# Kernel tuning notes

Measured on AMD Instinct MI355X. Metric: run time of the kernel, lower is better.

Reference implementation:

```python
import jax, jax.numpy as jnp
import numpy as np

B, S, D, H = 2, 4096, 512, 8
DK = D // H  # 64

def setup_inputs() -> dict:
    key = jax.random.key(0)
    k1, k2, k3, k4 = jax.random.split(key, 4)
    return {
        "queries": jax.random.normal(k1, (B, S, D), dtype=jnp.float32),
        "keys": jax.random.normal(k2, (B, S, D), dtype=jnp.float32),
        "values": jax.random.normal(k3, (B, S, D), dtype=jnp.float32),
        "W_o": jax.random.normal(k4, (D, D), dtype=jnp.float32) * (1.0 / np.sqrt(D)),
        "b_o": jnp.zeros((D,), dtype=jnp.float32),
    }

def reference(queries, keys, values, W_o, b_o):
    b_s, nq, _ = queries.shape
    nk = keys.shape[1]
    # split heads: (b, s, h, dk) -> (b, h, s, dk)
    q = queries.reshape(b_s, nq, H, DK).transpose(0, 2, 1, 3)
    k = keys.reshape(b_s, nk, H, DK).transpose(0, 2, 1, 3)
    v = values.reshape(b_s, nk, H, DK).transpose(0, 2, 1, 3)
    # full (nq, nk) attention matrix, scaled by sqrt(d_k)
    att = jnp.einsum("bhqd,bhkd->bhqk", q, k) / np.sqrt(DK).astype(np.float32)
    att = jax.nn.softmax(att, axis=-1)  # dropout is identity at inference
    out = jnp.einsum("bhqk,bhkd->bhqd", att, v)
    out = out.transpose(0, 2, 1, 3).reshape(b_s, nq, H * DK)
    return out @ W_o + b_o
```

## Files before the change

### kernel.cpp

```cpp
#include <hip/hip_runtime.h>
#include <hip/hip_bf16.h>

#define Bn 2
#define Sn 4096
#define Dn 512
#define Hn 8
#define DKn 64

typedef __bf16 bf16x8 __attribute__((ext_vector_type(8)));
typedef float f32x16 __attribute__((ext_vector_type(16)));

static __device__ __forceinline__ unsigned short f2bf(float x) {
    __hip_bfloat16 h = __float2bfloat16(x);
    return *reinterpret_cast<unsigned short*>(&h);
}

static __device__ __forceinline__ uint2 pack4(float a, float b, float c, float d) {
    union { ushort4 u; uint2 v; } r;
    r.u.x = f2bf(a); r.u.y = f2bf(b); r.u.z = f2bf(c); r.u.w = f2bf(d);
    return r.v;
}

static __device__ __forceinline__ bf16x8 xchg_frag(uint2 pg0, uint2 pg1, int hi) {
    int sx = hi ? (int)pg0.x : (int)pg1.x;
    int sy = hi ? (int)pg0.y : (int)pg1.y;
    int rx = __shfl_xor(sx, 32);
    int ry = __shfl_xor(sy, 32);
    unsigned ox = hi ? pg1.x : pg0.x;
    unsigned oy = hi ? pg1.y : pg0.y;
    union { unsigned u[4]; bf16x8 v; } f;
    f.u[0] = hi ? (unsigned)rx : ox;
    f.u[1] = hi ? (unsigned)ry : oy;
    f.u[2] = hi ? ox : (unsigned)rx;
    f.u[3] = hi ? oy : (unsigned)ry;
    return f.v;
}

__global__ __launch_bounds__(256) void kprep_kernel(const float* __restrict__ K,
                                                    unsigned short* __restrict__ Kb) {
    const int kt = blockIdx.x, bh = blockIdx.y;
    const int b = bh >> 3, h = bh & 7;
    unsigned short* dst = Kb + ((size_t)bh * 64 + kt) * 4096;
#pragma unroll
    for (int i = 0; i < 2; ++i) {
        int c = threadIdx.x + i * 256;
        int f = c >> 6, ln = c & 63;
        int ktile = f >> 2, ks = f & 3;
        int row = ktile * 32 + (ln & 31);
        int dk = ks * 16 + (ln >> 5) * 8;
        const float* src = K + ((size_t)(b * Sn + kt * 64 + row)) * Dn + h * 64 + dk;
        float4 a0 = *(const float4*)src;
        float4 a1 = *(const float4*)(src + 4);
        ushort4 o0; o0.x = f2bf(a0.x); o0.y = f2bf(a0.y); o0.z = f2bf(a0.z); o0.w = f2bf(a0.w);
        ushort4 o1; o1.x = f2bf(a1.x); o1.y = f2bf(a1.y); o1.z = f2bf(a1.z); o1.w = f2bf(a1.w);
        *(ushort4*)(dst + c * 8) = o0;
        *(ushort4*)(dst + c * 8 + 4) = o1;
    }
}

__global__ __launch_bounds__(256) void vprep_kernel(const float* __restrict__ V,
                                                    unsigned short* __restrict__ Vb) {
    const int kt = blockIdx.x, bh = blockIdx.y;
    const int b = bh >> 3, h = bh & 7;
    unsigned short* dst = Vb + ((size_t)bh * 64 + kt) * 4096;
#pragma unroll
    for (int i = 0; i < 2; ++i) {
        int c = threadIdx.x + i * 256;
        int f = c >> 6, ln = c & 63;
        int dt = f >> 2, ks = f & 3;
        int dk = dt * 32 + (ln & 31);
        int key0 = ks * 16 + (ln >> 5) * 8;
        const float* src = V + ((size_t)(b * Sn + kt * 64 + key0)) * Dn + h * 64 + dk;
        ushort4 o0, o1;
        o0.x = f2bf(src[0 * Dn]); o0.y = f2bf(src[1 * Dn]);
        o0.z = f2bf(src[2 * Dn]); o0.w = f2bf(src[3 * Dn]);
        o1.x = f2bf(src[4 * Dn]); o1.y = f2bf(src[5 * Dn]);
        o1.z = f2bf(src[6 * Dn]); o1.w = f2bf(src[7 * Dn]);
        *(ushort4*)(dst + c * 8) = o0;
        *(ushort4*)(dst + c * 8 + 4) = o1;
    }
}

__global__ __launch_bounds__(256) void wprep_kernel(const float* __restrict__ W,
                                                    unsigned short* __restrict__ Wb) {
    int c = blockIdx.x * 256 + threadIdx.x;
    int ln = c & 63, f = c >> 6;
    int ntile = f >> 5, ks = f & 31;
    int n = ntile * 32 + (ln & 31);
    int k0 = ks * 16 + (ln >> 5) * 8;
    ushort4 o0, o1;
    o0.x = f2bf(W[(size_t)(k0 + 0) * Dn + n]); o0.y = f2bf(W[(size_t)(k0 + 1) * Dn + n]);
    o0.z = f2bf(W[(size_t)(k0 + 2) * Dn + n]); o0.w = f2bf(W[(size_t)(k0 + 3) * Dn + n]);
    o1.x = f2bf(W[(size_t)(k0 + 4) * Dn + n]); o1.y = f2bf(W[(size_t)(k0 + 5) * Dn + n]);
    o1.z = f2bf(W[(size_t)(k0 + 6) * Dn + n]); o1.w = f2bf(W[(size_t)(k0 + 7) * Dn + n]);
    *(ushort4*)(Wb + c * 8) = o0;
    *(ushort4*)(Wb + c * 8 + 4) = o1;
}

__global__ __launch_bounds__(256) void attn_kernel(
    const float* __restrict__ Q,
    const unsigned short* __restrict__ Kb,
    const unsigned short* __restrict__ Vb,
    unsigned short* __restrict__ ObA) {
    __shared__ __align__(16) unsigned short Ksh[4096];
    __shared__ __align__(16) unsigned short Vsh[4096];

    const int qt = blockIdx.x;
    const int bh = blockIdx.y;
    const int b = bh >> 3, h = bh & 7;
    const int tid = threadIdx.x;
    const int w = tid >> 6;
    const int lane = tid & 63;
    const int q = lane & 31;
    const int hi = lane >> 5;
    const int q0 = qt * 128 + w * 32;
    const float cexp = 0.18033688f;

    bf16x8 qf[4];
    {
        const float* qp = Q + ((size_t)(b * Sn + q0 + q)) * Dn + h * 64 + hi * 8;
#pragma unroll
        for (int ks = 0; ks < 4; ++ks) {
            float4 a0 = *(const float4*)(qp + ks * 16);
            float4 a1 = *(const float4*)(qp + ks * 16 + 4);
            union { unsigned short u[8]; bf16x8 v; } f;
            f.u[0] = f2bf(a0.x * cexp); f.u[1] = f2bf(a0.y * cexp);
            f.u[2] = f2bf(a0.z * cexp); f.u[3] = f2bf(a0.w * cexp);
            f.u[4] = f2bf(a1.x * cexp); f.u[5] = f2bf(a1.y * cexp);
            f.u[6] = f2bf(a1.z * cexp); f.u[7] = f2bf(a1.w * cexp);
            qf[ks] = f.v;
        }
    }

    f32x16 oacc[2];
#pragma unroll
    for (int t = 0; t < 2; ++t)
#pragma unroll
        for (int r = 0; r < 16; ++r) oacc[t][r] = 0.f;
    float l_ = 0.f;

    const unsigned short* kg = Kb + (size_t)bh * (64 * 4096);
    const unsigned short* vg = Vb + (size_t)bh * (64 * 4096);

    for (int kt = 0; kt < 64; ++kt) {
        __syncthreads();
        {
            const unsigned short* ks_ = kg + (size_t)kt * 4096;
            const unsigned short* vs_ = vg + (size_t)kt * 4096;
            uint4 k0 = *(const uint4*)(ks_ + tid * 8);
            uint4 k1 = *(const uint4*)(ks_ + 2048 + tid * 8);
            uint4 v0 = *(const uint4*)(vs_ + tid * 8);
            uint4 v1 = *(const uint4*)(vs_ + 2048 + tid * 8);
            *(uint4*)&Ksh[tid * 8] = k0;
            *(uint4*)&Ksh[2048 + tid * 8] = k1;
            *(uint4*)&Vsh[tid * 8] = v0;
            *(uint4*)&Vsh[2048 + tid * 8] = v1;
        }
        __syncthreads();

        f32x16 sacc[2];
#pragma unroll
        for (int t = 0; t < 2; ++t)
#pragma unroll
            for (int r = 0; r < 16; ++r) sacc[t][r] = 0.f;
#pragma unroll
        for (int ks = 0; ks < 4; ++ks) {
            bf16x8 ka0 = *(const bf16x8*)&Ksh[(0 * 4 + ks) * 512 + lane * 8];
            bf16x8 ka1 = *(const bf16x8*)&Ksh[(1 * 4 + ks) * 512 + lane * 8];
            sacc[0] = __builtin_amdgcn_mfma_f32_32x32x16_bf16(ka0, qf[ks], sacc[0], 0, 0, 0);
            sacc[1] = __builtin_amdgcn_mfma_f32_32x32x16_bf16(ka1, qf[ks], sacc[1], 0, 0, 0);
        }

        float p[2][16];
#pragma unroll
        for (int t = 0; t < 2; ++t) {
            float s0 = 0.f, s1 = 0.f;
#pragma unroll
            for (int r = 0; r < 16; r += 2) {
                float e0 = __builtin_amdgcn_exp2f(sacc[t][r]);
                float e1 = __builtin_amdgcn_exp2f(sacc[t][r + 1]);
                p[t][r] = e0; p[t][r + 1] = e1;
                s0 += e0; s1 += e1;
            }
            l_ += s0 + s1;
        }

#pragma unroll
        for (int kp = 0; kp < 4; ++kp) {
            const int c = kp >> 1, k2 = kp & 1;
            uint2 pg0 = pack4(p[c][8 * k2 + 0], p[c][8 * k2 + 1], p[c][8 * k2 + 2], p[c][8 * k2 + 3]);
            uint2 pg1 = pack4(p[c][8 * k2 + 4], p[c][8 * k2 + 5], p[c][8 * k2 + 6], p[c][8 * k2 + 7]);
            bf16x8 pb = xchg_frag(pg0, pg1, hi);
            bf16x8 va0 = *(const bf16x8*)&Vsh[(0 * 4 + kp) * 512 + lane * 8];
            bf16x8 va1 = *(const bf16x8*)&Vsh[(1 * 4 + kp) * 512 + lane * 8];
            oacc[0] = __builtin_amdgcn_mfma_f32_32x32x16_bf16(va0, pb, oacc[0], 0, 0, 0);
            oacc[1] = __builtin_amdgcn_mfma_f32_32x32x16_bf16(va1, pb, oacc[1], 0, 0, 0);
        }
    }

    l_ += __shfl_xor(l_, 32);
    const float li = 1.f / l_;
    const int gm = b * 128 + qt * 4 + w;
#pragma unroll
    for (int ksg = 0; ksg < 4; ++ksg) {
        const int dt = ksg >> 1, k2 = ksg & 1;
        uint2 pg0 = pack4(oacc[dt][8 * k2 + 0] * li, oacc[dt][8 * k2 + 1] * li,
                          oacc[dt][8 * k2 + 2] * li, oacc[dt][8 * k2 + 3] * li);
        uint2 pg1 = pack4(oacc[dt][8 * k2 + 4] * li, oacc[dt][8 * k2 + 5] * li,
                          oacc[dt][8 * k2 + 6] * li, oacc[dt][8 * k2 + 7] * li);
        bf16x8 frag = xchg_frag(pg0, pg1, hi);
        union { bf16x8 v; uint4 u; } fu; fu.v = frag;
        *(uint4*)&ObA[((size_t)(gm * 32 + h * 4 + ksg) * 64 + lane) * 8] = fu.u;
    }
}

__global__ __launch_bounds__(256) void proj_kernel(
    const unsigned short* __restrict__ ObA,
    const unsigned short* __restrict__ Wb,
    const float* __restrict__ bias,
    float* __restrict__ out) {
    __shared__ __align__(16) unsigned short Ash[8192];
    __shared__ __align__(16) unsigned short Wsh[4096];

    const int mt = blockIdx.x;
    const int nt = blockIdx.y;
    const int tid = threadIdx.x;
    const int w = tid >> 6;
    const int lane = tid & 63;
    const int q = lane & 31;
    const int hi = lane >> 5;

    f32x16 acc[2];
#pragma unroll
    for (int t = 0; t < 2; ++t)
#pragma unroll
        for (int r = 0; r < 16; ++r) acc[t][r] = 0.f;

    for (int kt = 0; kt < 8; ++kt) {
        __syncthreads();
#pragma unroll
        for (int i = 0; i < 4; ++i) {
            int ci = (tid >> 6) + i * 4;
            int ml = ci >> 2, ksl = ci & 3;
            *(uint4*)&Ash[ci * 512 + lane * 8] =
                *(const uint4*)(ObA + (((size_t)(mt * 4 + ml) * 32 + kt * 4 + ksl) * 64 + lane) * 8);
        }
#pragma unroll
        for (int i = 0; i < 2; ++i) {
            int ci = (tid >> 6) + i * 4;
            int ntl = ci >> 2, ksl = ci & 3;
            *(uint4*)&Wsh[ci * 512 + lane * 8] =
                *(const uint4*)(Wb + (((size_t)(nt * 2 + ntl) * 32 + kt * 4 + ksl) * 64 + lane) * 8);
        }
        __syncthreads();

#pragma unroll
        for (int ks = 0; ks < 4; ++ks) {
            bf16x8 a  = *(const bf16x8*)&Ash[(w * 4 + ks) * 512 + lane * 8];
            bf16x8 b0 = *(const bf16x8*)&Wsh[(0 * 4 + ks) * 512 + lane * 8];
            bf16x8 b1 = *(const bf16x8*)&Wsh[(4 + ks) * 512 + lane * 8];
            acc[0] = __builtin_amdgcn_mfma_f32_32x32x16_bf16(a, b0, acc[0], 0, 0, 0);
            acc[1] = __builtin_amdgcn_mfma_f32_32x32x16_bf16(a, b1, acc[1], 0, 0, 0);
        }
    }

#pragma unroll
    for (int ntl = 0; ntl < 2; ++ntl) {
        int col = nt * 64 + ntl * 32 + q;
        float bv = bias[col];
#pragma unroll
        for (int reg = 0; reg < 16; ++reg) {
            int row = mt * 128 + w * 32 + (reg & 3) + 8 * (reg >> 2) + 4 * hi;
            out[(size_t)row * Dn + col] = acc[ntl][reg] + bv;
        }
    }
}

extern "C" void kernel_launch(void* const* d_in, const int* in_sizes, int n_in,
                              void* d_out, int out_size, void* d_ws, size_t ws_size,
                              hipStream_t stream) {
    const float* Q = (const float*)d_in[0];
    const float* K = (const float*)d_in[1];
    const float* V = (const float*)d_in[2];
    const float* W = (const float*)d_in[3];
    const float* bo = (const float*)d_in[4];
    float* out = (float*)d_out;

    char* ws = (char*)d_ws;
    unsigned short* Kb  = (unsigned short*)(ws);
    unsigned short* Vb  = (unsigned short*)(ws + 8388608);
    unsigned short* Wb  = (unsigned short*)(ws + 16777216);
    unsigned short* ObA = (unsigned short*)(ws + 17301504);

    kprep_kernel<<<dim3(64, 16), 256, 0, stream>>>(K, Kb);
    vprep_kernel<<<dim3(64, 16), 256, 0, stream>>>(V, Vb);
    wprep_kernel<<<128, 256, 0, stream>>>(W, Wb);
    attn_kernel<<<dim3(32, 16), 256, 0, stream>>>(Q, Kb, Vb, ObA);
    proj_kernel<<<dim3(64, 8), 256, 0, stream>>>(ObA, Wb, bo, out);
}
```

Baseline: 218.2 us.

## Split attention KV loop across two wave groups, fuse prep kernels, cheaper bf16 pack

The attention kernel now runs 512 threads per block, with two halves of four waves each. Each half processes half of the key tiles into its own LDS buffers, and the partial output accumulators and row sums are combined through LDS at the end. This doubles the waves working on each query tile, aiming at better latency hiding. The three prep kernels are merged into one launch to save launch overhead. Float-to-bf16 conversion now uses add-0x8000 plus a perm instruction; this is round-half-up rather than round-to-nearest-even and does not handle NaN specially.

```diff
diff --git a/kernel.cpp b/kernel.cpp
--- a/kernel.cpp
+++ b/kernel.cpp
@@ -5,29 +5,24 @@
 #define Sn 4096
 #define Dn 512
 #define Hn 8
-#define DKn 64
 
 typedef __bf16 bf16x8 __attribute__((ext_vector_type(8)));
 typedef float f32x16 __attribute__((ext_vector_type(16)));
 
-static __device__ __forceinline__ unsigned short f2bf(float x) {
-    __hip_bfloat16 h = __float2bfloat16(x);
-    return *reinterpret_cast<unsigned short*>(&h);
-}
-
-static __device__ __forceinline__ uint2 pack4(float a, float b, float c, float d) {
-    union { ushort4 u; uint2 v; } r;
-    r.u.x = f2bf(a); r.u.y = f2bf(b); r.u.z = f2bf(c); r.u.w = f2bf(d);
-    return r.v;
-}
-
-static __device__ __forceinline__ bf16x8 xchg_frag(uint2 pg0, uint2 pg1, int hi) {
-    int sx = hi ? (int)pg0.x : (int)pg1.x;
-    int sy = hi ? (int)pg0.y : (int)pg1.y;
+static __device__ __forceinline__ unsigned pk2(float a, float b) {
+    unsigned ua = __float_as_uint(a) + 0x8000u;
+    unsigned ub = __float_as_uint(b) + 0x8000u;
+    return __builtin_amdgcn_perm(ub, ua, 0x07060302u);
+}
+
+static __device__ __forceinline__ bf16x8 xchg2(unsigned g0x, unsigned g0y,
+                                               unsigned g1x, unsigned g1y, int hi) {
+    int sx = hi ? (int)g0x : (int)g1x;
+    int sy = hi ? (int)g0y : (int)g1y;
     int rx = __shfl_xor(sx, 32);
     int ry = __shfl_xor(sy, 32);
-    unsigned ox = hi ? pg1.x : pg0.x;
-    unsigned oy = hi ? pg1.y : pg0.y;
+    unsigned ox = hi ? g1x : g0x;
+    unsigned oy = hi ? g1y : g0y;
     union { unsigned u[4]; bf16x8 v; } f;
     f.u[0] = hi ? (unsigned)rx : ox;
     f.u[1] = hi ? (unsigned)ry : oy;
@@ -36,85 +31,88 @@
     return f.v;
 }
 
-__global__ __launch_bounds__(256) void kprep_kernel(const float* __restrict__ K,
-                                                    unsigned short* __restrict__ Kb) {
-    const int kt = blockIdx.x, bh = blockIdx.y;
-    const int b = bh >> 3, h = bh & 7;
-    unsigned short* dst = Kb + ((size_t)bh * 64 + kt) * 4096;
-#pragma unroll
-    for (int i = 0; i < 2; ++i) {
-        int c = threadIdx.x + i * 256;
-        int f = c >> 6, ln = c & 63;
-        int ktile = f >> 2, ks = f & 3;
-        int row = ktile * 32 + (ln & 31);
-        int dk = ks * 16 + (ln >> 5) * 8;
-        const float* src = K + ((size_t)(b * Sn + kt * 64 + row)) * Dn + h * 64 + dk;
-        float4 a0 = *(const float4*)src;
-        float4 a1 = *(const float4*)(src + 4);
-        ushort4 o0; o0.x = f2bf(a0.x); o0.y = f2bf(a0.y); o0.z = f2bf(a0.z); o0.w = f2bf(a0.w);
-        ushort4 o1; o1.x = f2bf(a1.x); o1.y = f2bf(a1.y); o1.z = f2bf(a1.z); o1.w = f2bf(a1.w);
-        *(ushort4*)(dst + c * 8) = o0;
-        *(ushort4*)(dst + c * 8 + 4) = o1;
-    }
-}
-
-__global__ __launch_bounds__(256) void vprep_kernel(const float* __restrict__ V,
-                                                    unsigned short* __restrict__ Vb) {
-    const int kt = blockIdx.x, bh = blockIdx.y;
-    const int b = bh >> 3, h = bh & 7;
-    unsigned short* dst = Vb + ((size_t)bh * 64 + kt) * 4096;
-#pragma unroll
-    for (int i = 0; i < 2; ++i) {
-        int c = threadIdx.x + i * 256;
-        int f = c >> 6, ln = c & 63;
-        int dt = f >> 2, ks = f & 3;
-        int dk = dt * 32 + (ln & 31);
-        int key0 = ks * 16 + (ln >> 5) * 8;
-        const float* src = V + ((size_t)(b * Sn + kt * 64 + key0)) * Dn + h * 64 + dk;
-        ushort4 o0, o1;
-        o0.x = f2bf(src[0 * Dn]); o0.y = f2bf(src[1 * Dn]);
-        o0.z = f2bf(src[2 * Dn]); o0.w = f2bf(src[3 * Dn]);
-        o1.x = f2bf(src[4 * Dn]); o1.y = f2bf(src[5 * Dn]);
-        o1.z = f2bf(src[6 * Dn]); o1.w = f2bf(src[7 * Dn]);
-        *(ushort4*)(dst + c * 8) = o0;
-        *(ushort4*)(dst + c * 8 + 4) = o1;
-    }
-}
-
-__global__ __launch_bounds__(256) void wprep_kernel(const float* __restrict__ W,
-                                                    unsigned short* __restrict__ Wb) {
-    int c = blockIdx.x * 256 + threadIdx.x;
-    int ln = c & 63, f = c >> 6;
-    int ntile = f >> 5, ks = f & 31;
-    int n = ntile * 32 + (ln & 31);
-    int k0 = ks * 16 + (ln >> 5) * 8;
-    ushort4 o0, o1;
-    o0.x = f2bf(W[(size_t)(k0 + 0) * Dn + n]); o0.y = f2bf(W[(size_t)(k0 + 1) * Dn + n]);
-    o0.z = f2bf(W[(size_t)(k0 + 2) * Dn + n]); o0.w = f2bf(W[(size_t)(k0 + 3) * Dn + n]);
-    o1.x = f2bf(W[(size_t)(k0 + 4) * Dn + n]); o1.y = f2bf(W[(size_t)(k0 + 5) * Dn + n]);
-    o1.z = f2bf(W[(size_t)(k0 + 6) * Dn + n]); o1.w = f2bf(W[(size_t)(k0 + 7) * Dn + n]);
-    *(ushort4*)(Wb + c * 8) = o0;
-    *(ushort4*)(Wb + c * 8 + 4) = o1;
-}
-
-__global__ __launch_bounds__(256) void attn_kernel(
+__global__ __launch_bounds__(256) void prep_kernel(
+    const float* __restrict__ K, const float* __restrict__ V, const float* __restrict__ W,
+    unsigned short* __restrict__ Kb, unsigned short* __restrict__ Vb,
+    unsigned short* __restrict__ Wb) {
+    const int vb = blockIdx.x;
+    const int tid = threadIdx.x;
+    if (vb < 1024) {
+        const int kt = vb & 63, bh = vb >> 6;
+        const int b = bh >> 3, h = bh & 7;
+        unsigned short* dst = Kb + ((size_t)bh * 64 + kt) * 4096;
+#pragma unroll
+        for (int i = 0; i < 2; ++i) {
+            int c = tid + i * 256;
+            int f = c >> 6, ln = c & 63;
+            int ktile = f >> 2, ks = f & 3;
+            int row = ktile * 32 + (ln & 31);
+            int dk = ks * 16 + (ln >> 5) * 8;
+            const float* src = K + ((size_t)(b * Sn + kt * 64 + row)) * Dn + h * 64 + dk;
+            float4 a0 = *(const float4*)src;
+            float4 a1 = *(const float4*)(src + 4);
+            uint4 o;
+            o.x = pk2(a0.x, a0.y); o.y = pk2(a0.z, a0.w);
+            o.z = pk2(a1.x, a1.y); o.w = pk2(a1.z, a1.w);
+            *(uint4*)(dst + c * 8) = o;
+        }
+    } else if (vb < 2048) {
+        const int u = vb - 1024;
+        const int kt = u & 63, bh = u >> 6;
+        const int b = bh >> 3, h = bh & 7;
+        unsigned short* dst = Vb + ((size_t)bh * 64 + kt) * 4096;
+#pragma unroll
+        for (int i = 0; i < 2; ++i) {
+            int c = tid + i * 256;
+            int f = c >> 6, ln = c & 63;
+            int dt = f >> 2, ks = f & 3;
+            int dk = dt * 32 + (ln & 31);
+            int key0 = ks * 16 + (ln >> 5) * 8;
+            const float* src = V + ((size_t)(b * Sn + kt * 64 + key0)) * Dn + h * 64 + dk;
+            uint4 o;
+            o.x = pk2(src[0 * Dn], src[1 * Dn]); o.y = pk2(src[2 * Dn], src[3 * Dn]);
+            o.z = pk2(src[4 * Dn], src[5 * Dn]); o.w = pk2(src[6 * Dn], src[7 * Dn]);
+            *(uint4*)(dst + c * 8) = o;
+        }
+    } else {
+        int c = (vb - 2048) * 256 + tid;
+        int ln = c & 63, f = c >> 6;
+        int ntile = f >> 5, ks = f & 31;
+        int n = ntile * 32 + (ln & 31);
+        int k0 = ks * 16 + (ln >> 5) * 8;
+        uint4 o;
+        o.x = pk2(W[(size_t)(k0 + 0) * Dn + n], W[(size_t)(k0 + 1) * Dn + n]);
+        o.y = pk2(W[(size_t)(k0 + 2) * Dn + n], W[(size_t)(k0 + 3) * Dn + n]);
+        o.z = pk2(W[(size_t)(k0 + 4) * Dn + n], W[(size_t)(k0 + 5) * Dn + n]);
+        o.w = pk2(W[(size_t)(k0 + 6) * Dn + n], W[(size_t)(k0 + 7) * Dn + n]);
+        *(uint4*)(Wb + c * 8) = o;
+    }
+}
+
+__global__ __launch_bounds__(512, 4) void attn_kernel(
     const float* __restrict__ Q,
     const unsigned short* __restrict__ Kb,
     const unsigned short* __restrict__ Vb,
     unsigned short* __restrict__ ObA) {
-    __shared__ __align__(16) unsigned short Ksh[4096];
-    __shared__ __align__(16) unsigned short Vsh[4096];
+    __shared__ __align__(16) unsigned short KV[16384];
+    __shared__ float Lsh[4][64];
 
     const int qt = blockIdx.x;
     const int bh = blockIdx.y;
     const int b = bh >> 3, h = bh & 7;
     const int tid = threadIdx.x;
-    const int w = tid >> 6;
+    const int wg = tid >> 6;
+    const int half = wg >> 2;
+    const int w4 = wg & 3;
     const int lane = tid & 63;
     const int q = lane & 31;
     const int hi = lane >> 5;
-    const int q0 = qt * 128 + w * 32;
+    const int q0 = qt * 128 + w4 * 32;
+    const int th = tid & 255;
     const float cexp = 0.18033688f;
+
+    unsigned short* Kbuf = KV + half * 4096;
+    unsigned short* Vbuf = KV + 8192 + half * 4096;
 
     bf16x8 qf[4];
     {
@@ -123,94 +121,115 @@
         for (int ks = 0; ks < 4; ++ks) {
             float4 a0 = *(const float4*)(qp + ks * 16);
             float4 a1 = *(const float4*)(qp + ks * 16 + 4);
-            union { unsigned short u[8]; bf16x8 v; } f;
-            f.u[0] = f2bf(a0.x * cexp); f.u[1] = f2bf(a0.y * cexp);
-            f.u[2] = f2bf(a0.z * cexp); f.u[3] = f2bf(a0.w * cexp);
-            f.u[4] = f2bf(a1.x * cexp); f.u[5] = f2bf(a1.y * cexp);
-            f.u[6] = f2bf(a1.z * cexp); f.u[7] = f2bf(a1.w * cexp);
+            union { unsigned u[4]; bf16x8 v; } f;
+            f.u[0] = pk2(a0.x * cexp, a0.y * cexp);
+            f.u[1] = pk2(a0.z * cexp, a0.w * cexp);
+            f.u[2] = pk2(a1.x * cexp, a1.y * cexp);
+            f.u[3] = pk2(a1.z * cexp, a1.w * cexp);
             qf[ks] = f.v;
         }
     }
 
+    f32x16 zf;
+#pragma unroll
+    for (int r = 0; r < 16; ++r) zf[r] = 0.f;
     f32x16 oacc[2];
-#pragma unroll
-    for (int t = 0; t < 2; ++t)
-#pragma unroll
-        for (int r = 0; r < 16; ++r) oacc[t][r] = 0.f;
+    oacc[0] = zf; oacc[1] = zf;
     float l_ = 0.f;
 
-    const unsigned short* kg = Kb + (size_t)bh * (64 * 4096);
-    const unsigned short* vg = Vb + (size_t)bh * (64 * 4096);
-
-    for (int kt = 0; kt < 64; ++kt) {
+    const size_t tbase = ((size_t)bh * 64 + half * 32) * 4096;
+    const unsigned short* kg = Kb + tbase;
+    const unsigned short* vg = Vb + tbase;
+
+    for (int it = 0; it < 32; ++it) {
         __syncthreads();
         {
-            const unsigned short* ks_ = kg + (size_t)kt * 4096;
-            const unsigned short* vs_ = vg + (size_t)kt * 4096;
-            uint4 k0 = *(const uint4*)(ks_ + tid * 8);
-            uint4 k1 = *(const uint4*)(ks_ + 2048 + tid * 8);
-            uint4 v0 = *(const uint4*)(vs_ + tid * 8);
-            uint4 v1 = *(const uint4*)(vs_ + 2048 + tid * 8);
-            *(uint4*)&Ksh[tid * 8] = k0;
-            *(uint4*)&Ksh[2048 + tid * 8] = k1;
-            *(uint4*)&Vsh[tid * 8] = v0;
-            *(uint4*)&Vsh[2048 + tid * 8] = v1;
+            const unsigned short* ks_ = kg + (size_t)it * 4096;
+            const unsigned short* vs_ = vg + (size_t)it * 4096;
+            uint4 k0v = *(const uint4*)(ks_ + th * 8);
+            uint4 k1v = *(const uint4*)(ks_ + 2048 + th * 8);
+            uint4 v0v = *(const uint4*)(vs_ + th * 8);
+            uint4 v1v = *(const uint4*)(vs_ + 2048 + th * 8);
+            *(uint4*)&Kbuf[th * 8] = k0v;
+            *(uint4*)&Kbuf[2048 + th * 8] = k1v;
+            *(uint4*)&Vbuf[th * 8] = v0v;
+            *(uint4*)&Vbuf[2048 + th * 8] = v1v;
         }
         __syncthreads();
 
-        f32x16 sacc[2];
-#pragma unroll
-        for (int t = 0; t < 2; ++t)
-#pragma unroll
-            for (int r = 0; r < 16; ++r) sacc[t][r] = 0.f;
-#pragma unroll
-        for (int ks = 0; ks < 4; ++ks) {
-            bf16x8 ka0 = *(const bf16x8*)&Ksh[(0 * 4 + ks) * 512 + lane * 8];
-            bf16x8 ka1 = *(const bf16x8*)&Ksh[(1 * 4 + ks) * 512 + lane * 8];
-            sacc[0] = __builtin_amdgcn_mfma_f32_32x32x16_bf16(ka0, qf[ks], sacc[0], 0, 0, 0);
-            sacc[1] = __builtin_amdgcn_mfma_f32_32x32x16_bf16(ka1, qf[ks], sacc[1], 0, 0, 0);
-        }
-
-        float p[2][16];
 #pragma unroll
         for (int t = 0; t < 2; ++t) {
+            bf16x8 ka = *(const bf16x8*)&Kbuf[(t * 4 + 0) * 512 + lane * 8];
+            f32x16 sa = __builtin_amdgcn_mfma_f32_32x32x16_bf16(ka, qf[0], zf, 0, 0, 0);
+#pragma unroll
+            for (int ks = 1; ks < 4; ++ks) {
+                ka = *(const bf16x8*)&Kbuf[(t * 4 + ks) * 512 + lane * 8];
+                sa = __builtin_amdgcn_mfma_f32_32x32x16_bf16(ka, qf[ks], sa, 0, 0, 0);
+            }
+            float e[16];
             float s0 = 0.f, s1 = 0.f;
 #pragma unroll
             for (int r = 0; r < 16; r += 2) {
-                float e0 = __builtin_amdgcn_exp2f(sacc[t][r]);
-                float e1 = __builtin_amdgcn_exp2f(sacc[t][r + 1]);
-                p[t][r] = e0; p[t][r + 1] = e1;
-                s0 += e0; s1 += e1;
+                e[r] = __builtin_amdgcn_exp2f(sa[r]);
+                e[r + 1] = __builtin_amdgcn_exp2f(sa[r + 1]);
+                s0 += e[r]; s1 += e[r + 1];
             }
             l_ += s0 + s1;
-        }
-
-#pragma unroll
-        for (int kp = 0; kp < 4; ++kp) {
-            const int c = kp >> 1, k2 = kp & 1;
-            uint2 pg0 = pack4(p[c][8 * k2 + 0], p[c][8 * k2 + 1], p[c][8 * k2 + 2], p[c][8 * k2 + 3]);
-            uint2 pg1 = pack4(p[c][8 * k2 + 4], p[c][8 * k2 + 5], p[c][8 * k2 + 6], p[c][8 * k2 + 7]);
-            bf16x8 pb = xchg_frag(pg0, pg1, hi);
-            bf16x8 va0 = *(const bf16x8*)&Vsh[(0 * 4 + kp) * 512 + lane * 8];
-            bf16x8 va1 = *(const bf16x8*)&Vsh[(1 * 4 + kp) * 512 + lane * 8];
-            oacc[0] = __builtin_amdgcn_mfma_f32_32x32x16_bf16(va0, pb, oacc[0], 0, 0, 0);
-            oacc[1] = __builtin_amdgcn_mfma_f32_32x32x16_bf16(va1, pb, oacc[1], 0, 0, 0);
-        }
-    }
-
-    l_ += __shfl_xor(l_, 32);
-    const float li = 1.f / l_;
-    const int gm = b * 128 + qt * 4 + w;
-#pragma unroll
-    for (int ksg = 0; ksg < 4; ++ksg) {
-        const int dt = ksg >> 1, k2 = ksg & 1;
-        uint2 pg0 = pack4(oacc[dt][8 * k2 + 0] * li, oacc[dt][8 * k2 + 1] * li,
-                          oacc[dt][8 * k2 + 2] * li, oacc[dt][8 * k2 + 3] * li);
-        uint2 pg1 = pack4(oacc[dt][8 * k2 + 4] * li, oacc[dt][8 * k2 + 5] * li,
-                          oacc[dt][8 * k2 + 6] * li, oacc[dt][8 * k2 + 7] * li);
-        bf16x8 frag = xchg_frag(pg0, pg1, hi);
-        union { bf16x8 v; uint4 u; } fu; fu.v = frag;
-        *(uint4*)&ObA[((size_t)(gm * 32 + h * 4 + ksg) * 64 + lane) * 8] = fu.u;
+#pragma unroll
+            for (int k2 = 0; k2 < 2; ++k2) {
+                unsigned g0x = pk2(e[8 * k2 + 0], e[8 * k2 + 1]);
+                unsigned g0y = pk2(e[8 * k2 + 2], e[8 * k2 + 3]);
+                unsigned g1x = pk2(e[8 * k2 + 4], e[8 * k2 + 5]);
+                unsigned g1y = pk2(e[8 * k2 + 6], e[8 * k2 + 7]);
+                bf16x8 pb = xchg2(g0x, g0y, g1x, g1y, hi);
+                const int kp = t * 2 + k2;
+                bf16x8 va0 = *(const bf16x8*)&Vbuf[(0 * 4 + kp) * 512 + lane * 8];
+                bf16x8 va1 = *(const bf16x8*)&Vbuf[(1 * 4 + kp) * 512 + lane * 8];
+                oacc[0] = __builtin_amdgcn_mfma_f32_32x32x16_bf16(va0, pb, oacc[0], 0, 0, 0);
+                oacc[1] = __builtin_amdgcn_mfma_f32_32x32x16_bf16(va1, pb, oacc[1], 0, 0, 0);
+            }
+        }
+    }
+
+    __syncthreads();
+    float* rp = (float*)KV + w4 * 2048;
+    if (half) {
+#pragma unroll
+        for (int g = 0; g < 8; ++g) {
+            float4 v;
+            v.x = oacc[g >> 2][(g & 3) * 4 + 0];
+            v.y = oacc[g >> 2][(g & 3) * 4 + 1];
+            v.z = oacc[g >> 2][(g & 3) * 4 + 2];
+            v.w = oacc[g >> 2][(g & 3) * 4 + 3];
+            *(float4*)&rp[g * 256 + lane * 4] = v;
+        }
+        Lsh[w4][lane] = l_;
+    }
+    __syncthreads();
+    if (!half) {
+#pragma unroll
+        for (int g = 0; g < 8; ++g) {
+            float4 v = *(const float4*)&rp[g * 256 + lane * 4];
+            oacc[g >> 2][(g & 3) * 4 + 0] += v.x;
+            oacc[g >> 2][(g & 3) * 4 + 1] += v.y;
+            oacc[g >> 2][(g & 3) * 4 + 2] += v.z;
+            oacc[g >> 2][(g & 3) * 4 + 3] += v.w;
+        }
+        l_ += Lsh[w4][lane];
+        l_ += __shfl_xor(l_, 32);
+        const float li = 1.f / l_;
+        const int gm = b * 128 + qt * 4 + w4;
+#pragma unroll
+        for (int ksg = 0; ksg < 4; ++ksg) {
+            const int dt = ksg >> 1, k2 = ksg & 1;
+            unsigned g0x = pk2(oacc[dt][8 * k2 + 0] * li, oacc[dt][8 * k2 + 1] * li);
+            unsigned g0y = pk2(oacc[dt][8 * k2 + 2] * li, oacc[dt][8 * k2 + 3] * li);
+            unsigned g1x = pk2(oacc[dt][8 * k2 + 4] * li, oacc[dt][8 * k2 + 5] * li);
+            unsigned g1y = pk2(oacc[dt][8 * k2 + 6] * li, oacc[dt][8 * k2 + 7] * li);
+            bf16x8 frag = xchg2(g0x, g0y, g1x, g1y, hi);
+            union { bf16x8 v; uint4 u; } fu; fu.v = frag;
+            *(uint4*)&ObA[((size_t)(gm * 32 + h * 4 + ksg) * 64 + lane) * 8] = fu.u;
+        }
     }
 }
 
@@ -292,9 +311,7 @@
     unsigned short* Wb  = (unsigned short*)(ws + 16777216);
     unsigned short* ObA = (unsigned short*)(ws + 17301504);
 
-    kprep_kernel<<<dim3(64, 16), 256, 0, stream>>>(K, Kb);
-    vprep_kernel<<<dim3(64, 16), 256, 0, stream>>>(V, Vb);
-    wprep_kernel<<<128, 256, 0, stream>>>(W, Wb);
-    attn_kernel<<<dim3(32, 16), 256, 0, stream>>>(Q, Kb, Vb, ObA);
+    prep_kernel<<<2176, 256, 0, stream>>>(K, V, W, Kb, Vb, Wb);
+    attn_kernel<<<dim3(32, 16), 512, 0, stream>>>(Q, Kb, Vb, ObA);
     proj_kernel<<<dim3(64, 8), 256, 0, stream>>>(ObA, Wb, bo, out);
 }
```

After: 193.5 us. -11.3%, faster.
